# Performance work log

Hardware: AMD Instinct MI355X
Metric: run time of the kernel (lower is better)

The kernel has to match this reference:

```python
import jax, jax.numpy as jnp
import numpy as np

B, C, H, W = 4, 256, 64, 64
C8 = C // 8


def setup_inputs() -> dict:
    key = jax.random.key(0)
    ks = jax.random.split(key, 8)
    s = 1.0 / np.sqrt(C)
    return {
        "x_ccd": jax.random.normal(ks[0], (B, C, H, W), jnp.float32),
        "x_dem": jax.random.normal(ks[1], (B, C, H, W), jnp.float32),
        "Wq": jax.random.normal(ks[2], (C8, C), jnp.float32) * s,
        "bq": jax.random.normal(ks[3], (C8,), jnp.float32) * 0.01,
        "Wk": jax.random.normal(ks[4], (C8, C), jnp.float32) * s,
        "bk": jax.random.normal(ks[5], (C8,), jnp.float32) * 0.01,
        "Wv": jax.random.normal(ks[6], (C, C), jnp.float32) * s,
        "bv": jax.random.normal(ks[7], (C,), jnp.float32) * 0.01,
        "gamma": jnp.zeros((1,), jnp.float32),
    }


def reference(x_ccd, x_dem, Wq, bq, Wk, bk, Wv, bv, gamma):
    b, c, h, w = x_ccd.shape
    n = h * w
    xc = x_ccd.reshape(b, c, n)  # [B,C,N]
    xd = x_dem.reshape(b, c, n)
    # 1x1 convs == per-pixel linear projections
    q = jnp.einsum("oc,bcn->bno", Wq, xc) + bq  # [B,N,C8]
    k = jnp.einsum("oc,bcn->bon", Wk, xd) + bk[None, :, None]  # [B,C8,N]
    energy = jnp.einsum("bno,bom->bnm", q, k)  # [B,N,N]
    attention = jax.nn.softmax(energy, axis=-1)
    v = jnp.einsum("oc,bcn->bon", Wv, xd) + bv[None, :, None]  # [B,C,N]
    out = jnp.einsum("bom,bnm->bon", v, attention)  # value @ attention^T
    out = out.reshape(b, c, h, w)
    return gamma * out + x_ccd
```

## Files before the change

### kernel.cpp

```cpp
#include <hip/hip_runtime.h>

typedef unsigned short u16;
typedef unsigned int u32;
typedef short v8s __attribute__((ext_vector_type(8)));
typedef float v16f __attribute__((ext_vector_type(16)));

#define MFMA(a, b, c) __builtin_amdgcn_mfma_f32_32x32x16_bf16(a, b, c, 0, 0, 0)
#define L2E 1.44269504088896f

union U8 { v8s s; uint4 u4; u32 u[4]; };

__device__ __forceinline__ u16 f2bf(float x) {
    u32 u = __float_as_uint(x);
    return (u16)((u + 0x7FFFu + ((u >> 16) & 1u)) >> 16);
}
__device__ __forceinline__ u32 pk2(float a, float b) {
    return (u32)f2bf(a) | ((u32)f2bf(b) << 16);
}
__device__ __forceinline__ u32 pkz(float e0, float e1) {
    return __builtin_amdgcn_perm(__float_as_uint(e1), __float_as_uint(e0), 0x07060302u);
}


__global__ __launch_bounds__(256) void prep_w_kernel(
    const float* __restrict__ Wq, const float* __restrict__ bq,
    const float* __restrict__ Wk, const float* __restrict__ bk,
    const float* __restrict__ Wv, const float* __restrict__ bv,
    u16* __restrict__ WfT, float* __restrict__ ball)
{
    int tid = blockIdx.x * 256 + threadIdx.x;
    if (tid < 81920) {
        int ch = tid >> 8, c = tid & 255;
        float w;
        if (ch < 32)      w = Wq[ch * 256 + c];
        else if (ch < 64) w = Wk[(ch - 32) * 256 + c] * L2E;
        else              w = Wv[(ch - 64) * 256 + c];
        int tile = (ch >> 5) * 16 + (c >> 4);
        int lane = ((c >> 3) & 1) * 32 + (ch & 31);
        WfT[tile * 512 + lane * 8 + (c & 7)] = f2bf(w);
    } else if (tid < 82240) {
        int i = tid - 81920;
        float bb;
        if (i < 32)      bb = bq[i];
        else if (i < 64) bb = bk[i - 32] * L2E;
        else             bb = bv[i - 64];
        ball[i] = bb;
    }
}

__global__ __launch_bounds__(256, 2) void proj_kernel(
    const float* __restrict__ xc, const float* __restrict__ xd,
    const u16* __restrict__ WfT, const float* __restrict__ ball,
    u16* __restrict__ qfT, u16* __restrict__ kfT, u16* __restrict__ vfT)
{
    __shared__ u16 xls[2][32][264];
    int blk = blockIdx.x, b = blk >> 7, n0 = (blk & 127) * 32;
    int t = threadIdx.x, lane = t & 63, wv = t >> 6;
    int hl = lane >> 5, l31 = lane & 31;

#pragma unroll
    for (int p = 0; p < 4; p++) {
        int s = p * 256 + t;
        int arr = s >> 9, c4 = (s >> 3) & 63, n4s = s & 7;
        const float* src = arr ? xd : xc;
        size_t g0 = ((size_t)(b * 256 + c4 * 4)) * 4096 + n0 + n4s * 4;
        float4 r0 = *(const float4*)&src[g0];
        float4 r1 = *(const float4*)&src[g0 + 4096];
        float4 r2 = *(const float4*)&src[g0 + 8192];
        float4 r3 = *(const float4*)&src[g0 + 12288];
        *(uint2*)&xls[arr][n4s * 4 + 0][c4 * 4] = make_uint2(pk2(r0.x, r1.x), pk2(r2.x, r3.x));
        *(uint2*)&xls[arr][n4s * 4 + 1][c4 * 4] = make_uint2(pk2(r0.y, r1.y), pk2(r2.y, r3.y));
        *(uint2*)&xls[arr][n4s * 4 + 2][c4 * 4] = make_uint2(pk2(r0.z, r1.z), pk2(r2.z, r3.z));
        *(uint2*)&xls[arr][n4s * 4 + 3][c4 * 4] = make_uint2(pk2(r0.w, r1.w), pk2(r2.w, r3.w));
    }
    __syncthreads();

    int jobs[3];
    int nj;
    if (wv == 0)      { jobs[0] = 0; jobs[1] = 2; jobs[2] = 0; nj = 2; }
    else if (wv == 1) { jobs[0] = 1; jobs[1] = 3; jobs[2] = 0; nj = 2; }
    else if (wv == 2) { jobs[0] = 4; jobs[1] = 5; jobs[2] = 6; nj = 3; }
    else              { jobs[0] = 7; jobs[1] = 8; jobs[2] = 9; nj = 3; }

    int nt = blk & 127;
    int n = n0 + l31;
    int vl = ((n >> 3) & 1) * 32, tk = n >> 4, j8 = n & 7;

    for (int jj = 0; jj < nj; jj++) {
        int j = jobs[jj];
        int arr = (j != 0);
        const u16* wb = WfT + (size_t)(j * 16) * 512 + lane * 8;
        v16f acc = {};
#pragma unroll
        for (int kc = 0; kc < 16; kc++) {
            U8 bx, a;
            bx.u4 = *(const uint4*)&xls[arr][l31][kc * 16 + hl * 8];
            a.u4  = *(const uint4*)(wb + (size_t)kc * 512);
            acc = MFMA(a.s, bx.s, acc);
        }
        if (j <= 1) {
            u16* dst = j ? kfT : qfT;
#pragma unroll
            for (int i = 0; i < 8; i++) {
                int r = 2 * i;
                int row = (r & 3) + 8 * (r >> 2) + 4 * hl;
                float b0 = ball[j * 32 + row], b1 = ball[j * 32 + row + 1];
                u32 st = pk2(acc[r] + b0, acc[r + 1] + b1);
                size_t off = (((size_t)(b * 128 + nt) * 2 + (row >> 4)) * 512)
                           + (((row >> 3) & 1) * 32 + l31) * 8 + (row & 7);
                *(u32*)&dst[off] = st;
            }
        } else {
            int vi = j - 2;
            u16* vdst = vfT + (((size_t)(b * 8 + vi) * 256 + tk) * 512) + vl * 8 + j8;
#pragma unroll
            for (int r = 0; r < 16; r++) {
                int row = (r & 3) + 8 * (r >> 2) + 4 * hl;
                vdst[row * 8] = f2bf(acc[r] + ball[64 + vi * 32 + row]);
            }
        }
    }
}

__global__ __launch_bounds__(512, 2) void flash_kernel(
    const u16* __restrict__ qfT, const u16* __restrict__ kfT,
    const u16* __restrict__ vfT, const float* __restrict__ xccd,
    const float* __restrict__ gptr, float* __restrict__ outp)
{
    __shared__ float red[2][2][4][16][64];
    __shared__ float lred[2][2][32];

    const int t = threadIdx.x, lane = t & 63, wv = t >> 6;
    const int hl = lane >> 5, l31 = lane & 31;
    const int blk = blockIdx.x;
    const int b = (blk & 7) >> 1;
    const int qt = ((blk >> 3) << 1) | (blk & 1);
    const int kh = wv & 1, chh = (wv >> 1) & 1, qh = wv >> 2;
    const int n0 = qt * 64 + qh * 32;
    const int chbase = chh * 128;

    U8 qf0, qf1;
    {
        const u16* qp = qfT + ((size_t)(b * 128 + (n0 >> 5)) * 2) * 512 + lane * 8;
        qf0.u4 = *(const uint4*)qp;
        qf1.u4 = *(const uint4*)(qp + 512);
    }
    U8 ones;
#pragma unroll
    for (int i = 0; i < 8; i++) ones.s[i] = (short)0x3F80;

    v16f acc[4] = {};
    v16f lac = {};

    const u16* kbase = kfT + ((size_t)b * 128 * 2) * 512 + lane * 8;
    const u16* vbase = vfT + ((size_t)(b * 8 + chh * 4) * 256) * 512 + lane * 8;

    U8 k0[2], k1[2], k2[2], v0[4][2], v1[4][2], v2[4][2];

    auto load_frags = [&](int it, U8 (&kf)[2], U8 (&vf)[4][2]) {
        const int kt = it * 2 + kh;
        kf[0].u4 = *(const uint4*)(kbase + (size_t)(kt * 2) * 512);
        kf[1].u4 = *(const uint4*)(kbase + (size_t)(kt * 2 + 1) * 512);
        const int tk = it * 4 + kh * 2;
#pragma unroll
        for (int ct = 0; ct < 4; ct++) {
            const u16* vp = vbase + ((size_t)(ct * 256 + tk)) * 512;
            vf[ct][0].u4 = *(const uint4*)vp;
            vf[ct][1].u4 = *(const uint4*)(vp + 512);
        }
    };

    load_frags(0, k0, v0);
    load_frags(1, k1, v1);

    auto step = [&](int it, U8 (&kf)[2], U8 (&vf)[4][2], U8 (&kn)[2], U8 (&vn)[4][2]) {
        if (it + 2 < 64) load_frags(it + 2, kn, vn);
        v16f E = {};
        E = MFMA(kf[0].s, qf0.s, E);
        E = MFMA(kf[1].s, qf1.s, E);
        u32 pkv[8];
#pragma unroll
        for (int j = 0; j < 8; j++)
            pkv[j] = pkz(exp2f(E[2 * j]), exp2f(E[2 * j + 1]));
#pragma unroll
        for (int kc = 0; kc < 2; kc++) {
            const int pb = kc * 4;
            u32 p01 = pkv[pb], p23 = pkv[pb + 1];
            u32 p45 = pkv[pb + 2], p67 = pkv[pb + 3];
            u32 s0 = hl ? p01 : p45;
            u32 s1 = hl ? p23 : p67;
            u32 r0 = (u32)__shfl_xor((int)s0, 32, 64);
            u32 r1 = (u32)__shfl_xor((int)s1, 32, 64);
            U8 B;
            B.u[0] = hl ? r0 : p01;
            B.u[1] = hl ? r1 : p23;
            B.u[2] = hl ? p45 : r0;
            B.u[3] = hl ? p67 : r1;
            if (chh == 0) lac = MFMA(ones.s, B.s, lac);
#pragma unroll
            for (int ct = 0; ct < 4; ct++)
                acc[ct] = MFMA(vf[ct][kc].s, B.s, acc[ct]);
        }
    };
#pragma unroll 1
    for (int base = 0; base < 63; base += 3) {
        step(base,     k0, v0, k2, v2);
        step(base + 1, k1, v1, k0, v0);
        step(base + 2, k2, v2, k1, v1);
    }
    step(63, k0, v0, k1, v1);

    if (chh == 0 && lane < 32) lred[qh][kh][l31] = lac[0];
    if (kh == 1) {
#pragma unroll
        for (int ct = 0; ct < 4; ct++)
#pragma unroll
            for (int r = 0; r < 16; r++)
                red[qh][chh][ct][r][lane] = acc[ct][r];
    }
    __syncthreads();
    if (kh == 0) {
        const float g = gptr[0];
        const float sc = g / (lred[qh][0][l31] + lred[qh][1][l31]);
#pragma unroll
        for (int ct = 0; ct < 4; ct++)
#pragma unroll
            for (int r = 0; r < 16; r++) {
                float v = acc[ct][r] + red[qh][chh][ct][r][lane];
                int ch = chbase + ct * 32 + (r & 3) + 8 * (r >> 2) + 4 * hl;
                size_t ga = ((size_t)(b * 256 + ch)) * 4096 + n0 + l31;
                outp[ga] = v * sc + xccd[ga];
            }
    }
}

extern "C" void kernel_launch(void* const* d_in, const int* in_sizes, int n_in,
                              void* d_out, int out_size, void* d_ws, size_t ws_size,
                              hipStream_t stream)
{
    const float* xc    = (const float*)d_in[0];
    const float* xd    = (const float*)d_in[1];
    const float* Wq    = (const float*)d_in[2];
    const float* bq    = (const float*)d_in[3];
    const float* Wk    = (const float*)d_in[4];
    const float* bk    = (const float*)d_in[5];
    const float* Wv    = (const float*)d_in[6];
    const float* bv    = (const float*)d_in[7];
    const float* gamma = (const float*)d_in[8];
    float* out = (float*)d_out;

    u16* qfT  = (u16*)d_ws;
    u16* kfT  = qfT + (size_t)524288;
    u16* vfT  = kfT + (size_t)524288;
    u16* WfT  = vfT + (size_t)4194304;
    float* bl = (float*)(WfT + 81920);

    prep_w_kernel<<<322, 256, 0, stream>>>(Wq, bq, Wk, bk, Wv, bv, WfT, bl);
    proj_kernel<<<512, 256, 0, stream>>>(xc, xd, WfT, bl, qfT, kfT, vfT);
    flash_kernel<<<256, 512, 0, stream>>>(qfT, kfT, vfT, xc, gamma, out);
}
```

Measured before the change: 170.7 us.

## Software-pipeline QK MFMA one step ahead and use permlane32 swap for P

Computes the QK energy tile for the next iteration during the current step, so the exp2/pack work overlaps with MFMA issue instead of waiting on the QK result. It replaces the shfl_xor-and-select exchange of packed probabilities with permlane32_swap, uses the raw hardware exp2, and raises wave priority around the MFMA block. In exchange it keeps an extra live v16f energy register set, which raises register pressure and could hurt occupancy.

Measured after the change: 162.9 us. 4.6% less time.

```diff
diff --git a/kernel.cpp b/kernel.cpp
--- a/kernel.cpp
+++ b/kernel.cpp
@@ -4,6 +4,7 @@
 typedef unsigned int u32;
 typedef short v8s __attribute__((ext_vector_type(8)));
 typedef float v16f __attribute__((ext_vector_type(16)));
+typedef unsigned int v2u __attribute__((ext_vector_type(2)));
 
 #define MFMA(a, b, c) __builtin_amdgcn_mfma_f32_32x32x16_bf16(a, b, c, 0, 0, 0)
 #define L2E 1.44269504088896f
@@ -173,42 +174,58 @@
     load_frags(0, k0, v0);
     load_frags(1, k1, v1);
 
-    auto step = [&](int it, U8 (&kf)[2], U8 (&vf)[4][2], U8 (&kn)[2], U8 (&vn)[4][2]) {
+    v16f Ecur;
+    {
+        v16f E = {};
+        E = MFMA(k0[0].s, qf0.s, E);
+        E = MFMA(k0[1].s, qf1.s, E);
+        Ecur = E;
+    }
+
+    auto step = [&](int it, U8 (&kf)[2], U8 (&vf)[4][2], U8 (&kn)[2], U8 (&vn)[4][2],
+                    U8 (&knx)[2], bool doqk) {
         if (it + 2 < 64) load_frags(it + 2, kn, vn);
-        v16f E = {};
-        E = MFMA(kf[0].s, qf0.s, E);
-        E = MFMA(kf[1].s, qf1.s, E);
+
         u32 pkv[8];
 #pragma unroll
         for (int j = 0; j < 8; j++)
-            pkv[j] = pkz(exp2f(E[2 * j]), exp2f(E[2 * j + 1]));
-#pragma unroll
-        for (int kc = 0; kc < 2; kc++) {
-            const int pb = kc * 4;
-            u32 p01 = pkv[pb], p23 = pkv[pb + 1];
-            u32 p45 = pkv[pb + 2], p67 = pkv[pb + 3];
-            u32 s0 = hl ? p01 : p45;
-            u32 s1 = hl ? p23 : p67;
-            u32 r0 = (u32)__shfl_xor((int)s0, 32, 64);
-            u32 r1 = (u32)__shfl_xor((int)s1, 32, 64);
-            U8 B;
-            B.u[0] = hl ? r0 : p01;
-            B.u[1] = hl ? r1 : p23;
-            B.u[2] = hl ? p45 : r0;
-            B.u[3] = hl ? p67 : r1;
-            if (chh == 0) lac = MFMA(ones.s, B.s, lac);
-#pragma unroll
-            for (int ct = 0; ct < 4; ct++)
-                acc[ct] = MFMA(vf[ct][kc].s, B.s, acc[ct]);
-        }
+            pkv[j] = pkz(__builtin_amdgcn_exp2f(Ecur[2 * j]),
+                         __builtin_amdgcn_exp2f(Ecur[2 * j + 1]));
+        U8 B0, B1;
+        {
+            v2u r;
+            r = __builtin_amdgcn_permlane32_swap(pkv[0], pkv[2], 0, 0); B0.u[0] = r[0]; B0.u[2] = r[1];
+            r = __builtin_amdgcn_permlane32_swap(pkv[1], pkv[3], 0, 0); B0.u[1] = r[0]; B0.u[3] = r[1];
+            r = __builtin_amdgcn_permlane32_swap(pkv[4], pkv[6], 0, 0); B1.u[0] = r[0]; B1.u[2] = r[1];
+            r = __builtin_amdgcn_permlane32_swap(pkv[5], pkv[7], 0, 0); B1.u[1] = r[0]; B1.u[3] = r[1];
+        }
+
+        __builtin_amdgcn_s_setprio(1);
+        if (doqk) {
+            v16f E = {};
+            E = MFMA(knx[0].s, qf0.s, E);
+            E = MFMA(knx[1].s, qf1.s, E);
+            Ecur = E;
+        }
+        if (chh == 0) {
+            lac = MFMA(ones.s, B0.s, lac);
+            lac = MFMA(ones.s, B1.s, lac);
+        }
+#pragma unroll
+        for (int ct = 0; ct < 4; ct++) {
+            acc[ct] = MFMA(vf[ct][0].s, B0.s, acc[ct]);
+            acc[ct] = MFMA(vf[ct][1].s, B1.s, acc[ct]);
+        }
+        __builtin_amdgcn_s_setprio(0);
     };
+
 #pragma unroll 1
     for (int base = 0; base < 63; base += 3) {
-        step(base,     k0, v0, k2, v2);
-        step(base + 1, k1, v1, k0, v0);
-        step(base + 2, k2, v2, k1, v1);
-    }
-    step(63, k0, v0, k1, v1);
+        step(base,     k0, v0, k2, v2, k1, true);
+        step(base + 1, k1, v1, k0, v0, k2, true);
+        step(base + 2, k2, v2, k1, v1, k0, true);
+    }
+    step(63, k0, v0, k1, v1, k1, false);
 
     if (chh == 0 && lane < 32) lred[qh][kh][l31] = lac[0];
     if (kh == 1) {
```
